# Optimization experiments

Measured on AMD Instinct MI355X. Metric: run time of the kernel, lower is better.

The kernel has to match this reference:

```python
import jax, jax.numpy as jnp
import numpy as np

EPS = 1e-5

def _layernorm(x, g, b):
    mu = jnp.mean(x, axis=-1, keepdims=True)
    var = jnp.mean(jnp.square(x - mu), axis=-1, keepdims=True)
    return (x - mu) * jax.lax.rsqrt(var + EPS) * g + b

def setup_inputs() -> dict:
    key = jax.random.key(0)
    ks = jax.random.split(key, 12)
    B, S, D, F = 2, 2048, 1024, 4096
    w = lambda k, shp: jax.random.normal(k, shp, dtype=jnp.float32) * 0.02
    return {
        "x":  jax.random.normal(ks[0], (B, S, D), dtype=jnp.float32),
        "Wq": w(ks[1], (D, D)), "bq": jnp.zeros((D,), jnp.float32),
        "Wk": w(ks[2], (D, D)), "bk": jnp.zeros((D,), jnp.float32),
        "Wv": w(ks[3], (D, D)), "bv": jnp.zeros((D,), jnp.float32),
        "W1": w(ks[4], (F, D)), "b1": jnp.zeros((F,), jnp.float32),
        "W2": w(ks[5], (D, F)), "b2": jnp.zeros((D,), jnp.float32),
        "g1": jnp.ones((D,), jnp.float32), "beta1": jnp.zeros((D,), jnp.float32),
        "g2": jnp.ones((D,), jnp.float32), "beta2": jnp.zeros((D,), jnp.float32),
    }

def reference(x, Wq, bq, Wk, bk, Wv, bv, W1, b1, W2, b2, g1, beta1, g2, beta2):
    B, S, D = x.shape
    H = 16
    dk = D // H
    # QKV projections (torch nn.Linear: y = x @ W.T + b)
    q = (x @ Wq.T + bq).reshape(B, S, H, dk).transpose(0, 2, 1, 3)  # [B,H,S,dk]
    k = (x @ Wk.T + bk).reshape(B, S, H, dk).transpose(0, 2, 1, 3)
    v = (x @ Wv.T + bv).reshape(B, S, H, dk).transpose(0, 2, 1, 3)
    # naive full attention (no mask, dropout=identity in eval)
    scores = jnp.einsum("bhqd,bhkd->bhqk", q, k) / jnp.sqrt(jnp.float32(dk))
    probs = jax.nn.softmax(scores, axis=-1)
    attn = jnp.einsum("bhqk,bhkd->bhqd", probs, v)  # [B,H,S,dk]
    attn_out = attn.transpose(0, 2, 1, 3).reshape(B, S, D)  # NOTE: no output proj (combine unused in source)
    # residual + LN1
    h = _layernorm(x + attn_out, g1, beta1)
    # FFN: linear2(relu(linear1(h)))
    ffn = jax.nn.relu(h @ W1.T + b1) @ W2.T + b2
    # residual + LN2
    return _layernorm(h + ffn, g2, beta2)
```

## Files before the change

### kernel.cpp

```cpp
#include <hip/hip_runtime.h>
#include <stdint.h>

typedef unsigned short u16;
typedef __bf16 bf16x8 __attribute__((ext_vector_type(8)));
typedef short s16x8 __attribute__((ext_vector_type(8)));
typedef float f32x4 __attribute__((ext_vector_type(4)));

union FragU { s16x8 s; bf16x8 b; uint4 u; };

__device__ __forceinline__ f32x4 mfma_bf16(s16x8 a, s16x8 b, f32x4 c) {
    FragU ua, ub; ua.s = a; ub.s = b;
    return __builtin_amdgcn_mfma_f32_16x16x32_bf16(ua.b, ub.b, c, 0, 0, 0);
}

__device__ __forceinline__ u16 f2bf(float f) {
    uint32_t u = __float_as_uint(f);
    u += 0x7fffu + ((u >> 16) & 1u);
    return (u16)(u >> 16);
}

__device__ __forceinline__ float bf2f(u16 u) {
    return __uint_as_float((uint32_t)u << 16);
}

__device__ __forceinline__ void gload_lds16(const void* g, void* l) {
    __builtin_amdgcn_global_load_lds((__attribute__((address_space(1))) void*)g,
                                     (__attribute__((address_space(3))) void*)l,
                                     16, 0, 0);
}

__device__ __forceinline__ void xcd_swz(int& bx, int& by, int& bz) {
    int nx = gridDim.x, ny = gridDim.y;
    int nwg = nx * ny * gridDim.z;
    int lin = blockIdx.x + nx * (blockIdx.y + ny * blockIdx.z);
    int cpx = nwg >> 3;
    int s = (lin & 7) * cpx + (lin >> 3);
    bx = s % nx; s /= nx;
    by = s % ny; bz = s / ny;
}

__global__ void k_cast(const float* __restrict__ in, u16* __restrict__ out, int n4) {
    int i = blockIdx.x * blockDim.x + threadIdx.x;
    int stride = gridDim.x * blockDim.x;
    for (; i < n4; i += stride) {
        float4 v = ((const float4*)in)[i];
        u16 us[4] = {f2bf(v.x), f2bf(v.y), f2bf(v.z), f2bf(v.w)};
        *(uint2*)(out + (size_t)i * 4) = *(uint2*)us;
    }
}

template<int RELU, int OUTMODE>
__device__ __forceinline__ void gemm_body(
    const u16* __restrict__ A, const u16* __restrict__ W,
    const float* __restrict__ bias, void* __restrict__ Cout,
    int M, int N, int K, int row0, int col0, int kbeg, int kend)
{
    __shared__ __align__(16) u16 As[128 * 64];
    __shared__ __align__(16) u16 Bs[128 * 64];

    const int tid  = threadIdx.x;
    const int wid  = tid >> 6;
    const int lane = tid & 63;
    const int g    = lane >> 4;
    const int cc   = lane & 15;
    const int wr   = wid >> 1;
    const int wc   = wid & 1;

    f32x4 zero = {0.f, 0.f, 0.f, 0.f};
    f32x4 acc[4][4];
#pragma unroll
    for (int i = 0; i < 4; i++)
#pragma unroll
        for (int j = 0; j < 4; j++) acc[i][j] = zero;

    const int srow = tid >> 3;
    const int scol = ((tid & 7) ^ (srow & 7)) * 8;
    const u16* gA0 = A + (size_t)(row0 + srow) * K + scol;
    const u16* gB0 = W + (size_t)(col0 + srow) * K + scol;
    u16* lA0 = &As[wid * 512];
    u16* lB0 = &Bs[wid * 512];

    const int xm = (cc & 7);

    for (int k0 = kbeg; k0 < kend; k0 += 64) {
#pragma unroll
        for (int j = 0; j < 4; j++)
            gload_lds16(gA0 + (size_t)(j * 32) * K + k0, lA0 + j * 2048);
#pragma unroll
        for (int j = 0; j < 4; j++)
            gload_lds16(gB0 + (size_t)(j * 32) * K + k0, lB0 + j * 2048);
        __syncthreads();

#pragma unroll
        for (int h = 0; h < 2; h++) {
            const int slot = ((h * 4 + g) ^ xm) * 8;
            s16x8 af[4], bf[4];
#pragma unroll
            for (int mi = 0; mi < 4; mi++)
                af[mi] = *(const s16x8*)&As[(wr * 64 + mi * 16 + cc) * 64 + slot];
#pragma unroll
            for (int ni = 0; ni < 4; ni++)
                bf[ni] = *(const s16x8*)&Bs[(wc * 64 + ni * 16 + cc) * 64 + slot];
#pragma unroll
            for (int mi = 0; mi < 4; mi++)
#pragma unroll
                for (int ni = 0; ni < 4; ni++)
                    acc[mi][ni] = mfma_bf16(af[mi], bf[ni], acc[mi][ni]);
        }
        __syncthreads();
    }

#pragma unroll
    for (int ni = 0; ni < 4; ni++) {
        int col = col0 + wc * 64 + ni * 16 + cc;
        float bvv = 0.f;
        if (OUTMODE != 2) bvv = bias[col];
#pragma unroll
        for (int mi = 0; mi < 4; mi++) {
            int row = row0 + wr * 64 + mi * 16 + g * 4;
#pragma unroll
            for (int r = 0; r < 4; r++) {
                float v = acc[mi][ni][r] + bvv;
                if (RELU) v = fmaxf(v, 0.f);
                size_t idx = (size_t)(row + r) * N + col;
                if (OUTMODE == 0) ((float*)Cout)[idx] = v;
                else              ((u16*)Cout)[idx] = f2bf(v);
            }
        }
    }
}

__global__ __launch_bounds__(256, 4) void k_gemm_qkv(
    const u16* __restrict__ A, const u16* __restrict__ Wq, const u16* __restrict__ Wk,
    const u16* __restrict__ Wv, const float* __restrict__ bq, const float* __restrict__ bk,
    const float* __restrict__ bv, u16* __restrict__ Q, u16* __restrict__ K,
    u16* __restrict__ V, int M, int N, int Kd)
{
    int bx, by, bz; xcd_swz(bx, by, bz);
    const u16* W; const float* bb; u16* out;
    if (bz == 0)      { W = Wq; bb = bq; out = Q; }
    else if (bz == 1) { W = Wk; bb = bk; out = K; }
    else              { W = Wv; bb = bv; out = V; }
    gemm_body<0, 1>(A, W, bb, out, M, N, Kd, by * 128, bx * 128, 0, Kd);
}

__global__ __launch_bounds__(256, 4) void k_gemm_relu_bf16(
    const u16* __restrict__ A, const u16* __restrict__ W, const float* __restrict__ bias,
    u16* __restrict__ C, int M, int N, int K)
{
    int bx, by, bz; xcd_swz(bx, by, bz);
    gemm_body<1, 1>(A, W, bias, C, M, N, K, by * 128, bx * 128, 0, K);
}

__global__ __launch_bounds__(256, 4) void k_gemm_part(
    const u16* __restrict__ A, const u16* __restrict__ W,
    u16* __restrict__ p0, u16* __restrict__ p1, u16* __restrict__ p2, u16* __restrict__ p3,
    int M, int N, int K)
{
    int bx, by, bz; xcd_swz(bx, by, bz);
    u16* out = (bz == 0) ? p0 : (bz == 1) ? p1 : (bz == 2) ? p2 : p3;
    gemm_body<0, 2>(A, W, nullptr, out, M, N, K, by * 128, bx * 128, bz * 1024, bz * 1024 + 1024);
}

__global__ __launch_bounds__(256) void k_transpose_v(const u16* __restrict__ V, u16* __restrict__ Vt)
{
    constexpr int S = 2048, Dm = 1024;
    __shared__ __align__(16) u16 tile[64][72];
    int s0 = blockIdx.x * 64;
    int h = blockIdx.y, b = blockIdx.z;
    int tid = threadIdx.x;
    int r = tid >> 2, ch = tid & 3;
    const u16* src = V + (size_t)(b * S + s0 + r) * Dm + h * 64;
    *(s16x8*)&tile[r][ch * 8]      = *(const s16x8*)(src + ch * 8);
    *(s16x8*)&tile[r][ch * 8 + 32] = *(const s16x8*)(src + ch * 8 + 32);
    __syncthreads();
    int dd = tid >> 2, kc = tid & 3;
    u16 tmp[16];
#pragma unroll
    for (int j = 0; j < 16; j++) tmp[j] = tile[kc * 16 + j][dd];
    u16* dst = Vt + ((size_t)(b * 16 + h) * 64 + dd) * S + s0 + kc * 16;
    *(s16x8*)dst       = *(const s16x8*)&tmp[0];
    *(s16x8*)(dst + 8) = *(const s16x8*)&tmp[8];
}

__global__ __launch_bounds__(512, 4) void k_flash(
    const u16* __restrict__ Q, const u16* __restrict__ Kb,
    const u16* __restrict__ Vt, float* __restrict__ O)
{
    constexpr int S = 2048, Dm = 1024, H = 16;
    constexpr int KVB = 128;
    constexpr float qsc = 0.125f * 1.44269504f;
    constexpr float MFIX = 8.0f;
    int bx, by, bz; xcd_swz(bx, by, bz);
    int qt = bx, h = by, b = bz;
    int tid = threadIdx.x, wid = tid >> 6, lane = tid & 63;
    int g = lane >> 4, cc = lane & 15;

    __shared__ __align__(16) u16 Ks[128 * 64];
    __shared__ __align__(16) u16 Vs[64 * 128];

    int q0 = qt * 128 + wid * 16;
    size_t base = (size_t)b * S * Dm + h * 64;

    FragU uq0, uq1, qs0, qs1;
    uq0.s = *(const s16x8*)(Q + base + (size_t)(q0 + cc) * Dm + g * 8);
    uq1.s = *(const s16x8*)(Q + base + (size_t)(q0 + cc) * Dm + 32 + g * 8);
#pragma unroll
    for (int e = 0; e < 8; e++) {
        qs0.b[e] = (__bf16)((float)uq0.b[e] * qsc);
        qs1.b[e] = (__bf16)((float)uq1.b[e] * qsc);
    }
    s16x8 qf0 = qs0.s, qf1 = qs1.s;

    f32x4 zero = {0.f, 0.f, 0.f, 0.f};
    f32x4 o[4];
#pragma unroll
    for (int t = 0; t < 4; t++) o[t] = zero;
    float l_run = 0.f;

    const int krow = tid >> 3;
    const int kcol = ((tid & 7) ^ (krow & 7)) * 8;
    const u16* kSrcBase = Kb + base + (size_t)krow * Dm + kcol;
    u16* kDst0 = &Ks[wid * 512];
    u16* kDst1 = kDst0 + 4096;

    const int vrow = tid >> 3;
    const int vch  = (tid & 7) * 8;
    const int xmv  = (vrow & 7) << 3;
    const int cb0  = ((vch >> 5) << 5) | (((vch >> 4) & 1) << 2) | (((vch >> 2) & 3) << 3);
    const int cb1  = cb0 + 64;
    const u16* vSrcBase = Vt + (size_t)(b * H + h) * 64 * S + (size_t)vrow * S;
    u16* vq0a = &Vs[(vrow * 128 + cb0) ^ xmv];
    u16* vq0b = &Vs[(vrow * 128 + cb0 + 8) ^ xmv];
    u16* vq1a = &Vs[(vrow * 128 + cb1) ^ xmv];
    u16* vq1b = &Vs[(vrow * 128 + cb1 + 8) ^ xmv];

    s16x8 vpre0 = *(const s16x8*)(vSrcBase + vch);
    s16x8 vpre1 = *(const s16x8*)(vSrcBase + 64 + vch);

    const int xm = cc & 7;

    for (int kv0 = 0; kv0 < S; kv0 += KVB) {
        __syncthreads();
        gload_lds16(kSrcBase + (size_t)kv0 * Dm,        kDst0);
        gload_lds16(kSrcBase + (size_t)(kv0 + 64) * Dm, kDst1);
        {
            FragU a0, a1; a0.s = vpre0; a1.s = vpre1;
            *(uint2*)vq0a = make_uint2(a0.u.x, a0.u.y);
            *(uint2*)vq0b = make_uint2(a0.u.z, a0.u.w);
            *(uint2*)vq1a = make_uint2(a1.u.x, a1.u.y);
            *(uint2*)vq1b = make_uint2(a1.u.z, a1.u.w);
        }
        __syncthreads();
        if (kv0 + KVB < S) {
            vpre0 = *(const s16x8*)(vSrcBase + kv0 + KVB + vch);
            vpre1 = *(const s16x8*)(vSrcBase + kv0 + KVB + 64 + vch);
        }

        f32x4 sacc[8];
#pragma unroll
        for (int t = 0; t < 8; t++) sacc[t] = zero;
        __builtin_amdgcn_s_setprio(1);
#pragma unroll
        for (int t = 0; t < 8; t++) {
            const u16* kr = &Ks[(t * 16 + cc) * 64];
            s16x8 kf0 = *(const s16x8*)(kr + ((0 + g) ^ xm) * 8);
            s16x8 kf1 = *(const s16x8*)(kr + ((4 + g) ^ xm) * 8);
            sacc[t] = mfma_bf16(kf0, qf0, sacc[t]);
            sacc[t] = mfma_bf16(kf1, qf1, sacc[t]);
        }
        __builtin_amdgcn_s_setprio(0);

        FragU pb[4];
#pragma unroll
        for (int t = 0; t < 8; t++)
#pragma unroll
            for (int r = 0; r < 4; r++) {
                float pv = __builtin_amdgcn_exp2f(sacc[t][r] - MFIX);
                l_run += pv;
                pb[t >> 1].b[(t & 1) * 4 + r] = (__bf16)pv;
            }

        __builtin_amdgcn_s_setprio(1);
#pragma unroll
        for (int td = 0; td < 4; td++) {
            const int rb = (td * 16 + cc) * 128;
#pragma unroll
            for (int kk = 0; kk < 4; kk++) {
                s16x8 vf = *(const s16x8*)&Vs[(rb + kk * 32 + g * 8) ^ (xm << 3)];
                o[td] = mfma_bf16(vf, pb[kk].s, o[td]);
            }
        }
        __builtin_amdgcn_s_setprio(0);
    }

    l_run += __shfl_xor(l_run, 16, 64);
    l_run += __shfl_xor(l_run, 32, 64);
    float inv = 1.f / l_run;
#pragma unroll
    for (int td = 0; td < 4; td++) {
        float4 st = {o[td][0] * inv, o[td][1] * inv, o[td][2] * inv, o[td][3] * inv};
        *(float4*)&O[(size_t)(b * S + q0 + cc) * Dm + h * 64 + td * 16 + g * 4] = st;
    }
}

template<int WRITE_BF>
__global__ __launch_bounds__(256) void k_ln(
    const float* __restrict__ A, const float* __restrict__ B,
    const float* __restrict__ gw, const float* __restrict__ bw,
    float* __restrict__ outf, u16* __restrict__ outb)
{
    constexpr int D = 1024;
    int row = blockIdx.x;
    int t = threadIdx.x;
    int lane = t & 63, wid = t >> 6;
    float4 va = ((const float4*)(A + (size_t)row * D))[t];
    float4 vb = ((const float4*)(B + (size_t)row * D))[t];
    float v0 = va.x + vb.x, v1 = va.y + vb.y, v2 = va.z + vb.z, v3 = va.w + vb.w;
    float sum = v0 + v1 + v2 + v3;
    float sq  = v0 * v0 + v1 * v1 + v2 * v2 + v3 * v3;
#pragma unroll
    for (int off = 1; off < 64; off <<= 1) {
        sum += __shfl_xor(sum, off, 64);
        sq  += __shfl_xor(sq,  off, 64);
    }
    __shared__ float s1[4], s2[4];
    if (lane == 0) { s1[wid] = sum; s2[wid] = sq; }
    __syncthreads();
    sum = s1[0] + s1[1] + s1[2] + s1[3];
    sq  = s2[0] + s2[1] + s2[2] + s2[3];
    float mu  = sum * (1.f / D);
    float var = sq * (1.f / D) - mu * mu;
    float rs  = rsqrtf(var + 1e-5f);
    float4 gv = ((const float4*)gw)[t];
    float4 bv = ((const float4*)bw)[t];
    float y0 = (v0 - mu) * rs * gv.x + bv.x;
    float y1 = (v1 - mu) * rs * gv.y + bv.y;
    float y2 = (v2 - mu) * rs * gv.z + bv.z;
    float y3 = (v3 - mu) * rs * gv.w + bv.w;
    float4 yo = {y0, y1, y2, y3};
    ((float4*)(outf + (size_t)row * D))[t] = yo;
    if (WRITE_BF) {
        u16 us[4] = {f2bf(y0), f2bf(y1), f2bf(y2), f2bf(y3)};
        *(uint2*)(outb + (size_t)row * D + t * 4) = *(uint2*)us;
    }
}

__global__ __launch_bounds__(256) void k_ln2(
    const float* __restrict__ A,
    const u16* __restrict__ p0, const u16* __restrict__ p1,
    const u16* __restrict__ p2, const u16* __restrict__ p3,
    const float* __restrict__ bias,
    const float* __restrict__ gw, const float* __restrict__ bw,
    float* __restrict__ outf)
{
    constexpr int D = 1024;
    int row = blockIdx.x;
    int t = threadIdx.x;
    int lane = t & 63, wid = t >> 6;
    size_t idx = (size_t)row * D + t * 4;
    float4 va = ((const float4*)(A + (size_t)row * D))[t];
    float4 bb = ((const float4*)bias)[t];
    float v0 = va.x + bb.x, v1 = va.y + bb.y, v2 = va.z + bb.z, v3 = va.w + bb.w;
    const u16* ps[4] = {p0, p1, p2, p3};
#pragma unroll
    for (int pi = 0; pi < 4; pi++) {
        uint2 q = *(const uint2*)(ps[pi] + idx);
        v0 += bf2f((u16)q.x);
        v1 += bf2f((u16)(q.x >> 16));
        v2 += bf2f((u16)q.y);
        v3 += bf2f((u16)(q.y >> 16));
    }
    float sum = v0 + v1 + v2 + v3;
    float sq  = v0 * v0 + v1 * v1 + v2 * v2 + v3 * v3;
#pragma unroll
    for (int off = 1; off < 64; off <<= 1) {
        sum += __shfl_xor(sum, off, 64);
        sq  += __shfl_xor(sq,  off, 64);
    }
    __shared__ float s1[4], s2[4];
    if (lane == 0) { s1[wid] = sum; s2[wid] = sq; }
    __syncthreads();
    sum = s1[0] + s1[1] + s1[2] + s1[3];
    sq  = s2[0] + s2[1] + s2[2] + s2[3];
    float mu  = sum * (1.f / D);
    float var = sq * (1.f / D) - mu * mu;
    float rs  = rsqrtf(var + 1e-5f);
    float4 gv = ((const float4*)gw)[t];
    float4 bv = ((const float4*)bw)[t];
    float4 yo = {(v0 - mu) * rs * gv.x + bv.x,
                 (v1 - mu) * rs * gv.y + bv.y,
                 (v2 - mu) * rs * gv.z + bv.z,
                 (v3 - mu) * rs * gv.w + bv.w};
    ((float4*)(outf + (size_t)row * D))[t] = yo;
}

extern "C" void kernel_launch(void* const* d_in, const int* in_sizes, int n_in,
                              void* d_out, int out_size, void* d_ws, size_t ws_size,
                              hipStream_t stream)
{
    constexpr int B = 2, S = 2048, D = 1024, F = 4096, H = 16;
    constexpr int M = B * S;
    const float* x   = (const float*)d_in[0];
    const float* Wq  = (const float*)d_in[1];
    const float* bq  = (const float*)d_in[2];
    const float* Wk  = (const float*)d_in[3];
    const float* bk  = (const float*)d_in[4];
    const float* Wv  = (const float*)d_in[5];
    const float* bv  = (const float*)d_in[6];
    const float* W1  = (const float*)d_in[7];
    const float* b1  = (const float*)d_in[8];
    const float* W2  = (const float*)d_in[9];
    const float* b2  = (const float*)d_in[10];
    const float* g1  = (const float*)d_in[11];
    const float* be1 = (const float*)d_in[12];
    const float* g2  = (const float*)d_in[13];
    const float* be2 = (const float*)d_in[14];
    float* out = (float*)d_out;

    char* ws = (char*)d_ws;
    size_t off = 0;
    auto alloc = [&](size_t bytes) {
        void* p = ws + off;
        off += (bytes + 255) & ~(size_t)255;
        return p;
    };
    u16* xb   = (u16*)alloc((size_t)M * D * 2);
    u16* wqb  = (u16*)alloc((size_t)D * D * 2);
    u16* wkb  = (u16*)alloc((size_t)D * D * 2);
    u16* wvb  = (u16*)alloc((size_t)D * D * 2);
    u16* w1b  = (u16*)alloc((size_t)F * D * 2);
    u16* w2b  = (u16*)alloc((size_t)D * F * 2);
    u16* Qb   = (u16*)alloc((size_t)M * D * 2);
    u16* Kbf  = (u16*)alloc((size_t)M * D * 2);
    u16* Vb   = (u16*)alloc((size_t)M * D * 2);
    u16* Vtb  = (u16*)alloc((size_t)M * D * 2);
    float* attn = (float*)alloc((size_t)M * D * 4);
    float* hf   = (float*)alloc((size_t)M * D * 4);
    u16* hb     = (u16*)alloc((size_t)M * D * 2);
    u16* ffn1   = Qb;
    u16* p0 = xb;
    u16* p1 = w1b;
    u16* p2 = (u16*)attn;
    u16* p3 = ((u16*)attn) + (size_t)M * D;

    dim3 blk(256);
    k_cast<<<dim3(512), blk, 0, stream>>>(x,  xb,  M * D / 4);
    k_cast<<<dim3(256), blk, 0, stream>>>(Wq, wqb, D * D / 4);
    k_cast<<<dim3(256), blk, 0, stream>>>(Wk, wkb, D * D / 4);
    k_cast<<<dim3(256), blk, 0, stream>>>(Wv, wvb, D * D / 4);
    k_cast<<<dim3(512), blk, 0, stream>>>(W1, w1b, F * D / 4);
    k_cast<<<dim3(512), blk, 0, stream>>>(W2, w2b, D * F / 4);

    k_gemm_qkv<<<dim3(D / 128, M / 128, 3), blk, 0, stream>>>(
        xb, wqb, wkb, wvb, bq, bk, bv, Qb, Kbf, Vb, M, D, D);
    k_transpose_v<<<dim3(S / 64, H, B), blk, 0, stream>>>(Vb, Vtb);
    k_flash<<<dim3(S / 128, H, B), dim3(512), 0, stream>>>(Qb, Kbf, Vtb, attn);
    k_ln<1><<<dim3(M), blk, 0, stream>>>(x, attn, g1, be1, hf, hb);
    k_gemm_relu_bf16<<<dim3(F / 128, M / 128), blk, 0, stream>>>(hb, w1b, b1, ffn1, M, F, D);
    k_gemm_part<<<dim3(D / 128, M / 128, 4), blk, 0, stream>>>(
        ffn1, w2b, p0, p1, p2, p3, M, D, F);
    k_ln2<<<dim3(M), blk, 0, stream>>>(hf, p0, p1, p2, p3, b2, g2, be2, out);
}
```

Before: 205.4 us.

## Fuse V transpose into GEMM epilogue, drop fp32 LN1 output, fold softmax offset

The V projection now writes its output directly in the head-transposed layout from the GEMM epilogue, which removes the separate transpose kernel and the round trip through an intermediate V buffer. LN1 writes only a bf16 result, and LN2 reads that bf16 residual instead of an fp32 copy, cutting memory traffic at some precision cost. In flash attention, the fixed max offset is folded into the MFMA accumulator's initial value, and the row sum is kept per lane in a vector accumulator. ffn1 gets its own workspace buffer instead of aliasing Qb.

After: 209.7 us. 1.02x slower.

```diff
diff --git a/kernel.cpp b/kernel.cpp
--- a/kernel.cpp
+++ b/kernel.cpp
@@ -115,33 +115,53 @@
         int col = col0 + wc * 64 + ni * 16 + cc;
         float bvv = 0.f;
         if (OUTMODE != 2) bvv = bias[col];
-#pragma unroll
-        for (int mi = 0; mi < 4; mi++) {
-            int row = row0 + wr * 64 + mi * 16 + g * 4;
-#pragma unroll
-            for (int r = 0; r < 4; r++) {
-                float v = acc[mi][ni][r] + bvv;
-                if (RELU) v = fmaxf(v, 0.f);
-                size_t idx = (size_t)(row + r) * N + col;
-                if (OUTMODE == 0) ((float*)Cout)[idx] = v;
-                else              ((u16*)Cout)[idx] = f2bf(v);
+        if (OUTMODE == 3) {
+            int head = col >> 6, dh = col & 63;
+#pragma unroll
+            for (int mi = 0; mi < 4; mi++) {
+                int row = row0 + wr * 64 + mi * 16 + g * 4;
+                int bb = row >> 11, sl = row & 2047;
+                u16 us[4];
+#pragma unroll
+                for (int r = 0; r < 4; r++) us[r] = f2bf(acc[mi][ni][r] + bvv);
+                *(uint2*)&((u16*)Cout)[(((size_t)(bb * 16 + head) * 64 + dh) << 11) + sl]
+                    = *(uint2*)us;
             }
-        }
-    }
-}
-
-__global__ __launch_bounds__(256, 4) void k_gemm_qkv(
+        } else {
+#pragma unroll
+            for (int mi = 0; mi < 4; mi++) {
+                int row = row0 + wr * 64 + mi * 16 + g * 4;
+#pragma unroll
+                for (int r = 0; r < 4; r++) {
+                    float v = acc[mi][ni][r] + bvv;
+                    if (RELU) v = fmaxf(v, 0.f);
+                    size_t idx = (size_t)(row + r) * N + col;
+                    if (OUTMODE == 0) ((float*)Cout)[idx] = v;
+                    else              ((u16*)Cout)[idx] = f2bf(v);
+                }
+            }
+        }
+    }
+}
+
+__global__ __launch_bounds__(256, 4) void k_gemm_qk(
     const u16* __restrict__ A, const u16* __restrict__ Wq, const u16* __restrict__ Wk,
-    const u16* __restrict__ Wv, const float* __restrict__ bq, const float* __restrict__ bk,
-    const float* __restrict__ bv, u16* __restrict__ Q, u16* __restrict__ K,
-    u16* __restrict__ V, int M, int N, int Kd)
+    const float* __restrict__ bq, const float* __restrict__ bk,
+    u16* __restrict__ Q, u16* __restrict__ K, int M, int N, int Kd)
 {
     int bx, by, bz; xcd_swz(bx, by, bz);
-    const u16* W; const float* bb; u16* out;
-    if (bz == 0)      { W = Wq; bb = bq; out = Q; }
-    else if (bz == 1) { W = Wk; bb = bk; out = K; }
-    else              { W = Wv; bb = bv; out = V; }
+    const u16* W = (bz == 0) ? Wq : Wk;
+    const float* bb = (bz == 0) ? bq : bk;
+    u16* out = (bz == 0) ? Q : K;
     gemm_body<0, 1>(A, W, bb, out, M, N, Kd, by * 128, bx * 128, 0, Kd);
+}
+
+__global__ __launch_bounds__(256, 4) void k_gemm_vT(
+    const u16* __restrict__ A, const u16* __restrict__ Wv, const float* __restrict__ bv,
+    u16* __restrict__ Vt, int M, int N, int Kd)
+{
+    int bx, by, bz; xcd_swz(bx, by, bz);
+    gemm_body<0, 3>(A, Wv, bv, Vt, M, N, Kd, by * 128, bx * 128, 0, Kd);
 }
 
 __global__ __launch_bounds__(256, 4) void k_gemm_relu_bf16(
@@ -162,27 +182,6 @@
     gemm_body<0, 2>(A, W, nullptr, out, M, N, K, by * 128, bx * 128, bz * 1024, bz * 1024 + 1024);
 }
 
-__global__ __launch_bounds__(256) void k_transpose_v(const u16* __restrict__ V, u16* __restrict__ Vt)
-{
-    constexpr int S = 2048, Dm = 1024;
-    __shared__ __align__(16) u16 tile[64][72];
-    int s0 = blockIdx.x * 64;
-    int h = blockIdx.y, b = blockIdx.z;
-    int tid = threadIdx.x;
-    int r = tid >> 2, ch = tid & 3;
-    const u16* src = V + (size_t)(b * S + s0 + r) * Dm + h * 64;
-    *(s16x8*)&tile[r][ch * 8]      = *(const s16x8*)(src + ch * 8);
-    *(s16x8*)&tile[r][ch * 8 + 32] = *(const s16x8*)(src + ch * 8 + 32);
-    __syncthreads();
-    int dd = tid >> 2, kc = tid & 3;
-    u16 tmp[16];
-#pragma unroll
-    for (int j = 0; j < 16; j++) tmp[j] = tile[kc * 16 + j][dd];
-    u16* dst = Vt + ((size_t)(b * 16 + h) * 64 + dd) * S + s0 + kc * 16;
-    *(s16x8*)dst       = *(const s16x8*)&tmp[0];
-    *(s16x8*)(dst + 8) = *(const s16x8*)&tmp[8];
-}
-
 __global__ __launch_bounds__(512, 4) void k_flash(
     const u16* __restrict__ Q, const u16* __restrict__ Kb,
     const u16* __restrict__ Vt, float* __restrict__ O)
@@ -190,7 +189,6 @@
     constexpr int S = 2048, Dm = 1024, H = 16;
     constexpr int KVB = 128;
     constexpr float qsc = 0.125f * 1.44269504f;
-    constexpr float MFIX = 8.0f;
     int bx, by, bz; xcd_swz(bx, by, bz);
     int qt = bx, h = by, b = bz;
     int tid = threadIdx.x, wid = tid >> 6, lane = tid & 63;
@@ -212,11 +210,12 @@
     }
     s16x8 qf0 = qs0.s, qf1 = qs1.s;
 
+    f32x4 minit = {-8.f, -8.f, -8.f, -8.f};
     f32x4 zero = {0.f, 0.f, 0.f, 0.f};
     f32x4 o[4];
 #pragma unroll
     for (int t = 0; t < 4; t++) o[t] = zero;
-    float l_run = 0.f;
+    f32x4 lacc = zero;
 
     const int krow = tid >> 3;
     const int kcol = ((tid & 7) ^ (krow & 7)) * 8;
@@ -259,7 +258,7 @@
 
         f32x4 sacc[8];
 #pragma unroll
-        for (int t = 0; t < 8; t++) sacc[t] = zero;
+        for (int t = 0; t < 8; t++) sacc[t] = minit;
         __builtin_amdgcn_s_setprio(1);
 #pragma unroll
         for (int t = 0; t < 8; t++) {
@@ -276,8 +275,8 @@
         for (int t = 0; t < 8; t++)
 #pragma unroll
             for (int r = 0; r < 4; r++) {
-                float pv = __builtin_amdgcn_exp2f(sacc[t][r] - MFIX);
-                l_run += pv;
+                float pv = __builtin_amdgcn_exp2f(sacc[t][r]);
+                lacc[r] += pv;
                 pb[t >> 1].b[(t & 1) * 4 + r] = (__bf16)pv;
             }
 
@@ -294,6 +293,7 @@
         __builtin_amdgcn_s_setprio(0);
     }
 
+    float l_run = (lacc[0] + lacc[1]) + (lacc[2] + lacc[3]);
     l_run += __shfl_xor(l_run, 16, 64);
     l_run += __shfl_xor(l_run, 32, 64);
     float inv = 1.f / l_run;
@@ -304,11 +304,10 @@
     }
 }
 
-template<int WRITE_BF>
-__global__ __launch_bounds__(256) void k_ln(
+__global__ __launch_bounds__(256) void k_ln1(
     const float* __restrict__ A, const float* __restrict__ B,
     const float* __restrict__ gw, const float* __restrict__ bw,
-    float* __restrict__ outf, u16* __restrict__ outb)
+    u16* __restrict__ outb)
 {
     constexpr int D = 1024;
     int row = blockIdx.x;
@@ -334,20 +333,15 @@
     float rs  = rsqrtf(var + 1e-5f);
     float4 gv = ((const float4*)gw)[t];
     float4 bv = ((const float4*)bw)[t];
-    float y0 = (v0 - mu) * rs * gv.x + bv.x;
-    float y1 = (v1 - mu) * rs * gv.y + bv.y;
-    float y2 = (v2 - mu) * rs * gv.z + bv.z;
-    float y3 = (v3 - mu) * rs * gv.w + bv.w;
-    float4 yo = {y0, y1, y2, y3};
-    ((float4*)(outf + (size_t)row * D))[t] = yo;
-    if (WRITE_BF) {
-        u16 us[4] = {f2bf(y0), f2bf(y1), f2bf(y2), f2bf(y3)};
-        *(uint2*)(outb + (size_t)row * D + t * 4) = *(uint2*)us;
-    }
+    u16 us[4] = {f2bf((v0 - mu) * rs * gv.x + bv.x),
+                 f2bf((v1 - mu) * rs * gv.y + bv.y),
+                 f2bf((v2 - mu) * rs * gv.z + bv.z),
+                 f2bf((v3 - mu) * rs * gv.w + bv.w)};
+    *(uint2*)(outb + (size_t)row * D + t * 4) = *(uint2*)us;
 }
 
 __global__ __launch_bounds__(256) void k_ln2(
-    const float* __restrict__ A,
+    const u16* __restrict__ A,
     const u16* __restrict__ p0, const u16* __restrict__ p1,
     const u16* __restrict__ p2, const u16* __restrict__ p3,
     const float* __restrict__ bias,
@@ -359,9 +353,12 @@
     int t = threadIdx.x;
     int lane = t & 63, wid = t >> 6;
     size_t idx = (size_t)row * D + t * 4;
-    float4 va = ((const float4*)(A + (size_t)row * D))[t];
+    uint2 ha = *(const uint2*)(A + idx);
     float4 bb = ((const float4*)bias)[t];
-    float v0 = va.x + bb.x, v1 = va.y + bb.y, v2 = va.z + bb.z, v3 = va.w + bb.w;
+    float v0 = bf2f((u16)ha.x)         + bb.x;
+    float v1 = bf2f((u16)(ha.x >> 16)) + bb.y;
+    float v2 = bf2f((u16)ha.y)         + bb.z;
+    float v3 = bf2f((u16)(ha.y >> 16)) + bb.w;
     const u16* ps[4] = {p0, p1, p2, p3};
 #pragma unroll
     for (int pi = 0; pi < 4; pi++) {
@@ -433,12 +430,10 @@
     u16* w2b  = (u16*)alloc((size_t)D * F * 2);
     u16* Qb   = (u16*)alloc((size_t)M * D * 2);
     u16* Kbf  = (u16*)alloc((size_t)M * D * 2);
-    u16* Vb   = (u16*)alloc((size_t)M * D * 2);
     u16* Vtb  = (u16*)alloc((size_t)M * D * 2);
+    u16* ffn1 = (u16*)alloc((size_t)M * F * 2);
     float* attn = (float*)alloc((size_t)M * D * 4);
-    float* hf   = (float*)alloc((size_t)M * D * 4);
     u16* hb     = (u16*)alloc((size_t)M * D * 2);
-    u16* ffn1   = Qb;
     u16* p0 = xb;
     u16* p1 = w1b;
     u16* p2 = (u16*)attn;
@@ -452,13 +447,14 @@
     k_cast<<<dim3(512), blk, 0, stream>>>(W1, w1b, F * D / 4);
     k_cast<<<dim3(512), blk, 0, stream>>>(W2, w2b, D * F / 4);
 
-    k_gemm_qkv<<<dim3(D / 128, M / 128, 3), blk, 0, stream>>>(
-        xb, wqb, wkb, wvb, bq, bk, bv, Qb, Kbf, Vb, M, D, D);
-    k_transpose_v<<<dim3(S / 64, H, B), blk, 0, stream>>>(Vb, Vtb);
+    k_gemm_qk<<<dim3(D / 128, M / 128, 2), blk, 0, stream>>>(
+        xb, wqb, wkb, bq, bk, Qb, Kbf, M, D, D);
+    k_gemm_vT<<<dim3(D / 128, M / 128), blk, 0, stream>>>(
+        xb, wvb, bv, Vtb, M, D, D);
     k_flash<<<dim3(S / 128, H, B), dim3(512), 0, stream>>>(Qb, Kbf, Vtb, attn);
-    k_ln<1><<<dim3(M), blk, 0, stream>>>(x, attn, g1, be1, hf, hb);
+    k_ln1<<<dim3(M), blk, 0, stream>>>(x, attn, g1, be1, hb);
     k_gemm_relu_bf16<<<dim3(F / 128, M / 128), blk, 0, stream>>>(hb, w1b, b1, ffn1, M, F, D);
     k_gemm_part<<<dim3(D / 128, M / 128, 4), blk, 0, stream>>>(
         ffn1, w2b, p0, p1, p2, p3, M, D, F);
-    k_ln2<<<dim3(M), blk, 0, stream>>>(hf, p0, p1, p2, p3, b2, g2, be2, out);
-}
+    k_ln2<<<dim3(M), blk, 0, stream>>>(hb, p0, p1, p2, p3, b2, g2, be2, out);
+}
```
